# Kernel optimization log

Hardware: AMD Instinct MI355X
Metric: run time of the kernel (lower is better)

Reference implementation:

```python
import jax, jax.numpy as jnp
import numpy as np

B, N, DIM = 4, 8192, 1024
H, DH, W = 16, 64, 128
INNER = H * DH


def setup_inputs() -> dict:
    key = jax.random.key(0)
    k0, k1, k2, k3 = jax.random.split(key, 4)
    s = 0.02
    return {
        "x": jax.random.normal(k0, (B, N, DIM), jnp.float32),
        "wq": jax.random.normal(k1, (DIM, INNER), jnp.float32) * s,
        "wkv": jax.random.normal(k2, (DIM, 2 * INNER), jnp.float32) * s,
        "wo": jax.random.normal(k3, (INNER, DIM), jnp.float32) * s,
        "bo": jnp.zeros((DIM,), jnp.float32),
    }


def reference(x, wq, wkv, wo, bo):
    b, n, _ = x.shape
    h, dh, w = H, DH, W
    scale = dh ** -0.5
    # projections (n is a multiple of w, so no padding path)
    q = x @ wq
    k, v = jnp.split(x @ wkv, 2, axis=-1)

    def to_windows(t):
        # b n (h d) -> (b h) n d -> (b h) n/w w d
        t = t.reshape(b, n, h, dh).transpose(0, 2, 1, 3)
        return t.reshape(b * h, n // w, w, dh)

    qw, kw, vw = map(to_windows, (q, k, v))

    def add_prev_window(t):
        # prepend a zero window, then each window sees [prev, current] -> j = 2w
        tp = jnp.pad(t, ((0, 0), (1, 0), (0, 0), (0, 0)))
        return jnp.concatenate([tp[:, :-1], tp[:, 1:]], axis=2)

    kw, vw = add_prev_window(kw), add_prev_window(vw)

    sim = jnp.einsum('bwid,bwjd->bwij', qw, kw) * scale  # (bh, n/w, w, 2w)
    i, j = w, 2 * w
    causal = jnp.triu(jnp.ones((i, j), bool), j - i + 1)  # masks j > i + w
    neg = -jnp.finfo(sim.dtype).max
    sim = jnp.where(causal, neg, sim)
    attn = jax.nn.softmax(sim, axis=-1)
    out = jnp.einsum('bwij,bwjd->bwid', attn, vw)  # (bh, n/w, w, dh)
    out = out.reshape(b, h, n, dh).transpose(0, 2, 1, 3).reshape(b, n, h * dh)
    return out @ wo + bo
```

## Files before the change

### kernel.cpp

```cpp
#include <hip/hip_runtime.h>
#include <stdint.h>

typedef unsigned short u16;
typedef __bf16 bf16x8 __attribute__((ext_vector_type(8)));
typedef float f32x4 __attribute__((ext_vector_type(4)));
typedef unsigned short u16x8 __attribute__((ext_vector_type(8)));

#define MFMA16(a, b, c) __builtin_amdgcn_mfma_f32_16x16x32_bf16((a), (b), (c), 0, 0, 0)

#define SEQ_N 8192
#define NWIN 64

#define BAR() __builtin_amdgcn_s_barrier()
#define PRIO1() __builtin_amdgcn_s_setprio(1)
#define PRIO0() __builtin_amdgcn_s_setprio(0)
#define SB0() __builtin_amdgcn_sched_barrier(0)
#define VM8() asm volatile("s_waitcnt vmcnt(8)" ::: "memory")
#define VM0() asm volatile("s_waitcnt vmcnt(0)" ::: "memory")
#define LGKM0() asm volatile("s_waitcnt lgkmcnt(0)" ::: "memory")

__device__ __forceinline__ u16 f2bf(float f) {
  union { float f; uint32_t u; } v; v.f = f;
  return (u16)((v.u + 0x7fffu + ((v.u >> 16) & 1u)) >> 16);
}

__device__ __forceinline__ void load_lds16(const void* g, void* l) {
  __builtin_amdgcn_global_load_lds((const __attribute__((address_space(1))) void*)g,
                                   (__attribute__((address_space(3))) void*)l, 16, 0, 0);
}

__global__ __launch_bounds__(256) void cast_bf16_kernel(const float* __restrict__ src,
                                                        u16* __restrict__ dst, int n8) {
  int i = blockIdx.x * 256 + threadIdx.x;
  if (i >= n8) return;
  const float4* s = (const float4*)src + (size_t)i * 2;
  float4 a = s[0], b = s[1];
  u16x8 o;
  o[0] = f2bf(a.x); o[1] = f2bf(a.y); o[2] = f2bf(a.z); o[3] = f2bf(a.w);
  o[4] = f2bf(b.x); o[5] = f2bf(b.y); o[6] = f2bf(b.z); o[7] = f2bf(b.w);
  *((u16x8*)dst + i) = o;
}

__global__ __launch_bounds__(256) void transpose_cast_kernel(u16* __restrict__ dst,
                                                             const float* __restrict__ srcA,
                                                             const float* __restrict__ srcB,
                                                             int bcols) {
  __shared__ float tile[32][33];
  const int tx = threadIdx.x & 31, ty = threadIdx.x >> 5;
  const int n0 = blockIdx.x * 32, k0 = blockIdx.y * 32;
#pragma unroll
  for (int i = 0; i < 4; ++i) {
    int k = k0 + ty + i * 8;
    int n = n0 + tx;
    float v = (n < 1024) ? srcA[(size_t)k * 1024 + n]
                         : srcB[(size_t)k * bcols + (n - 1024)];
    tile[ty + i * 8][tx] = v;
  }
  __syncthreads();
#pragma unroll
  for (int i = 0; i < 4; ++i) {
    int n = n0 + ty + i * 8;
    int k = k0 + tx;
    dst[(size_t)n * 1024 + k] = f2bf(tile[tx][ty + i * 8]);
  }
}

#define READ_A_TO(dst, MH)                                                         \
  _Pragma("unroll") for (int kk = 0; kk < 2; ++kk)                                 \
  _Pragma("unroll") for (int m = 0; m < 4; ++m)                                    \
    dst[m][kk] = *(const bf16x8*)(Ard + bo + (((MH) * 64 + m * 16) << 7) + ax[kk]);

#define READ_B_TO(dst, NH)                                                         \
  _Pragma("unroll") for (int kk = 0; kk < 2; ++kk)                                 \
  _Pragma("unroll") for (int n = 0; n < 2; ++n)                                    \
    dst[n][kk] = *(const bf16x8*)(Brd + bo + (((NH) * 32 + n * 16) << 7) + ax[kk]);

#define MFMAQ(fa, fb, MH, NH)                                                      \
  _Pragma("unroll") for (int kk = 0; kk < 2; ++kk)                                 \
  _Pragma("unroll") for (int m = 0; m < 4; ++m)                                    \
  _Pragma("unroll") for (int n = 0; n < 2; ++n)                                    \
    acc[(MH) * 4 + m][(NH) * 2 + n] =                                              \
        MFMA16(fa[m][kk], fb[n][kk], acc[(MH) * 4 + m][(NH) * 2 + n]);

template <int NBN, int MODE>
__global__ __launch_bounds__(512, 2) void gemm8_kernel(
    const u16* __restrict__ A, const u16* __restrict__ Bt,
    u16* __restrict__ qo, u16* __restrict__ ko, u16* __restrict__ vo,
    float* __restrict__ out, const float* __restrict__ bias) {
  extern __shared__ char smem[];
  constexpr int K = 1024;
  constexpr int NT = K / 64;
  const int tid = threadIdx.x;
  const int wave = tid >> 6, lane = tid & 63;
  const int quad = lane >> 4, l15 = lane & 15;
  const int wm = wave >> 2, wn = wave & 3;

  const int idx0 = blockIdx.x;
  const int local = idx0 >> 3;
  const int bn = local >> 4;
  const int bm = ((idx0 & 7) << 4) + (local & 15);

  char* const Ab = smem;
  char* const Bb = smem + 65536;

  const int sr = lane >> 3;
  const int sg = ((lane & 7) ^ sr) * 8;
  const u16* const gA = A + (size_t)(bm * 256 + wave * 32 + sr) * K + sg;
  const u16* const gB = Bt + (size_t)(bn * 256 + wave * 32 + sr) * K + sg;
  const size_t aN = (size_t)((bm & 31) * 256 + wave * 32 + sr);
  const int ab16 = (bm >> 5) * 16;
  char* const lA = Ab + wave * 32 * 128;
  char* const lB = Bb + wave * 32 * 128;

  auto stage = [&](int buf, int kt) {
    if constexpr (MODE == 0) {
#pragma unroll
      for (int i = 0; i < 4; ++i)
        load_lds16(gA + (size_t)kt * 64 + i * 8 * K, lA + buf * 32768 + i * 1024);
    } else {
      const u16* g = A + (((size_t)(ab16 + kt)) << 19) + (aN << 6) + sg;
#pragma unroll
      for (int i = 0; i < 4; ++i)
        load_lds16(g + i * 512, lA + buf * 32768 + i * 1024);
    }
#pragma unroll
    for (int i = 0; i < 4; ++i)
      load_lds16(gB + (size_t)kt * 64 + i * 8 * K, lB + buf * 32768 + i * 1024);
  };

  const int ax[2] = { (quad ^ (l15 & 7)) << 4, ((quad ^ (l15 & 7)) << 4) ^ 64 };
  const char* const Ard = Ab + ((wm * 128 + l15) << 7);
  const char* const Brd = Bb + ((wn * 64 + l15) << 7);

  f32x4 acc[8][4] = {};
  bf16x8 afA[4][2], afB[4][2], bf0[2][2], bf1[2][2];

  stage(0, 0);
  stage(1, 1);
  VM8();
  BAR();

  for (int kt = 0; kt < NT; ++kt) {
    const int bo = (kt & 1) * 32768;
    READ_A_TO(afA, 0)
    READ_B_TO(bf0, 0)
    READ_B_TO(bf1, 1)
    SB0();
    PRIO1(); MFMAQ(afA, bf0, 0, 0) PRIO0();
    BAR();
    READ_A_TO(afB, 1)
    SB0();
    PRIO1(); MFMAQ(afA, bf1, 0, 1) PRIO0();
    BAR();
    PRIO1(); MFMAQ(afB, bf1, 1, 1) PRIO0();
    LGKM0();
    BAR();
    if (kt + 2 < NT) stage(kt & 1, kt + 2);
    PRIO1(); MFMAQ(afB, bf0, 1, 0) PRIO0();
    if (kt < NT - 1) {
      if (kt + 2 < NT) { VM8(); } else { VM0(); }
      BAR();
    }
  }

  const int row0 = bm * 256 + wm * 128;
#pragma unroll
  for (int mt = 0; mt < 8; ++mt) {
#pragma unroll
    for (int nt = 0; nt < 4; ++nt) {
      if (MODE == 0) {
        const int col = bn * 256 + wn * 64 + nt * 16 + l15;
        u16* dst = (col < 1024) ? qo : ((col < 2048) ? ko : vo);
        const int cc = col & 1023;
        const size_t hb = (((size_t)(ab16 + (cc >> 6))) << 19) + (size_t)(cc & 63);
        const int nb = (bm & 31) * 256 + wm * 128 + mt * 16 + quad * 4;
#pragma unroll
        for (int r = 0; r < 4; ++r)
          dst[hb + ((size_t)(nb + r) << 6)] = f2bf(acc[mt][nt][r]);
      } else {
        const int col = bn * 256 + wn * 64 + nt * 16 + l15;
        const float bv = bias[col];
#pragma unroll
        for (int r = 0; r < 4; ++r) {
          const int row = row0 + mt * 16 + quad * 4 + r;
          out[(size_t)row * 1024 + col] = acc[mt][nt][r] + bv;
        }
      }
    }
  }
}

__global__ __launch_bounds__(256, 2) void attn_kernel(const u16* __restrict__ qb,
                                                      const u16* __restrict__ kb,
                                                      const u16* __restrict__ vb,
                                                      u16* __restrict__ ob) {
  __shared__ u16 Vt[64][264];
  __shared__ u16 Ps[4 * 2048];
  const int tid = threadIdx.x;
  const int wave = tid >> 6, lane = tid & 63;
  const int quad = lane >> 4, l15 = lane & 15;
  const int raw = blockIdx.x;
  const int blk = ((raw & 7) << 9) | (raw >> 3);
  const int wi = blk & (NWIN - 1);
  const int bh = blk >> 6;
  const long qbase = ((long)bh * SEQ_N + (long)wi * 128) * 64;
  const long kbase = ((long)bh * SEQ_N + (long)wi * 128 - 128) * 64;

  {
    const int t = tid;
    const bool pad = (wi == 0) && (t < 128);
#pragma unroll
    for (int d0 = 0; d0 < 64; d0 += 8) {
      u16x8 v8;
      if (pad) {
        v8 = (u16x8)0;
      } else {
        v8 = *(const u16x8*)(vb + (kbase + (long)t * 64 + d0));
      }
#pragma unroll
      for (int j = 0; j < 8; ++j) Vt[d0 + j][t] = v8[j];
    }
  }

  bf16x8 qf[2][2];
#pragma unroll
  for (int mt = 0; mt < 2; ++mt)
#pragma unroll
    for (int kk = 0; kk < 2; ++kk)
      qf[mt][kk] = *(const bf16x8*)(qb + (qbase + (long)(wave * 32 + mt * 16 + l15) * 64 +
                                          kk * 32 + quad * 8));

  f32x4 s[2][16] = {};
#pragma unroll
  for (int nt = 0; nt < 16; ++nt) {
    if (!((wi == 0) && (nt < 8))) {
      const long kt = kbase + (long)(nt * 16 + l15) * 64;
      bf16x8 kf0 = *(const bf16x8*)(kb + (kt + quad * 8));
      bf16x8 kf1 = *(const bf16x8*)(kb + (kt + 32 + quad * 8));
#pragma unroll
      for (int mt = 0; mt < 2; ++mt) {
        s[mt][nt] = MFMA16(qf[mt][0], kf0, s[mt][nt]);
        s[mt][nt] = MFMA16(qf[mt][1], kf1, s[mt][nt]);
      }
    }
  }

#pragma unroll
  for (int mt = 0; mt < 2; ++mt) {
#pragma unroll
    for (int r = 0; r < 4; ++r) {
      const int row = wave * 32 + mt * 16 + quad * 4 + r;
      float m = -3.0e38f;
#pragma unroll
      for (int nt = 0; nt < 16; ++nt) {
        const int col = nt * 16 + l15;
        float x = s[mt][nt][r] * 0.125f;
        if (col > row + 128) x = -3.0e38f;
        s[mt][nt][r] = x;
        m = fmaxf(m, x);
      }
      m = fmaxf(m, __shfl_xor(m, 1));
      m = fmaxf(m, __shfl_xor(m, 2));
      m = fmaxf(m, __shfl_xor(m, 4));
      m = fmaxf(m, __shfl_xor(m, 8));
      float sum = 0.f;
#pragma unroll
      for (int nt = 0; nt < 16; ++nt) {
        float e = __expf(s[mt][nt][r] - m);
        s[mt][nt][r] = e;
        sum += e;
      }
      sum += __shfl_xor(sum, 1);
      sum += __shfl_xor(sum, 2);
      sum += __shfl_xor(sum, 4);
      sum += __shfl_xor(sum, 8);
      const float inv = 1.0f / sum;
#pragma unroll
      for (int nt = 0; nt < 16; ++nt) s[mt][nt][r] *= inv;
    }
  }

  __syncthreads();

  f32x4 o[2][4] = {};
#pragma unroll
  for (int ks = 0; ks < 8; ++ks) {
    u16* myP = &Ps[wave * 2048 + (ks & 1) * 1024];
#pragma unroll
    for (int mt = 0; mt < 2; ++mt)
#pragma unroll
      for (int half = 0; half < 2; ++half) {
        const int nt = ks * 2 + half;
#pragma unroll
        for (int r = 0; r < 4; ++r)
          myP[(mt * 16 + quad * 4 + r) * 32 + half * 16 + l15] = f2bf(s[mt][nt][r]);
      }
    bf16x8 pf[2];
    pf[0] = *(const bf16x8*)&myP[l15 * 32 + quad * 8];
    pf[1] = *(const bf16x8*)&myP[(16 + l15) * 32 + quad * 8];
#pragma unroll
    for (int ont = 0; ont < 4; ++ont) {
      bf16x8 vf = *(const bf16x8*)&Vt[ont * 16 + l15][ks * 32 + quad * 8];
      o[0][ont] = MFMA16(pf[0], vf, o[0][ont]);
      o[1][ont] = MFMA16(pf[1], vf, o[1][ont]);
    }
  }

#pragma unroll
  for (int mt = 0; mt < 2; ++mt)
#pragma unroll
    for (int ont = 0; ont < 4; ++ont)
#pragma unroll
      for (int r = 0; r < 4; ++r) {
        const int row = wave * 32 + mt * 16 + quad * 4 + r;
        const int col = ont * 16 + l15;
        ob[qbase + (long)row * 64 + col] = f2bf(o[mt][ont][r]);
      }
}

extern "C" void kernel_launch(void* const* d_in, const int* in_sizes, int n_in,
                              void* d_out, int out_size, void* d_ws, size_t ws_size,
                              hipStream_t stream) {
  const float* x   = (const float*)d_in[0];
  const float* wq  = (const float*)d_in[1];
  const float* wkv = (const float*)d_in[2];
  const float* wo  = (const float*)d_in[3];
  const float* bo  = (const float*)d_in[4];
  float* out = (float*)d_out;

  const size_t XE = (size_t)4 * SEQ_N * 1024;
  u16* ws = (u16*)d_ws;
  u16* xb    = ws;
  u16* qbuf  = ws + XE;
  u16* kbuf  = ws + 2 * XE;
  u16* vbuf  = ws + 3 * XE;
  u16* wqkvT = ws + 4 * XE;
  u16* woT   = wqkvT + 3072 * 1024;
  u16* obuf  = xb;

  hipFuncSetAttribute(reinterpret_cast<const void*>(gemm8_kernel<12, 0>),
                      hipFuncAttributeMaxDynamicSharedMemorySize, 131072);
  hipFuncSetAttribute(reinterpret_cast<const void*>(gemm8_kernel<4, 1>),
                      hipFuncAttributeMaxDynamicSharedMemorySize, 131072);

  cast_bf16_kernel<<<16384, 256, 0, stream>>>(x, xb, (int)(XE / 8));
  transpose_cast_kernel<<<dim3(96, 32), 256, 0, stream>>>(wqkvT, wq, wkv, 2048);
  transpose_cast_kernel<<<dim3(32, 32), 256, 0, stream>>>(woT, wo, wo, 1024);
  gemm8_kernel<12, 0><<<1536, 512, 131072, stream>>>(xb, wqkvT, qbuf, kbuf, vbuf,
                                                     nullptr, nullptr);
  attn_kernel<<<4096, 256, 0, stream>>>(qbuf, kbuf, vbuf, obuf);
  gemm8_kernel<4, 1><<<512, 512, 131072, stream>>>(obuf, woT, nullptr, nullptr, nullptr,
                                                   out, bo);
}
```

Baseline: 652.1 us.

## Stage K tile in LDS and XOR-swizzle V and P shared buffers

The attention kernel now copies the 256x64 K window into LDS once per block with direct global-to-LDS loads, instead of having every wave read K fragments from global memory. The padded V transpose buffer and the per-wave P staging buffer switch to XOR-swizzled layouts to cut LDS bank conflicts. The block barrier moves ahead of the QK^T loop. LDS use grows to about 80KB per block, which leaves only two blocks per CU, and the K copy for the first window now reads rows before the start of the tensor that are never used.

```diff
diff --git a/kernel.cpp b/kernel.cpp
--- a/kernel.cpp
+++ b/kernel.cpp
@@ -194,7 +194,8 @@
                                                       const u16* __restrict__ kb,
                                                       const u16* __restrict__ vb,
                                                       u16* __restrict__ ob) {
-  __shared__ u16 Vt[64][264];
+  __shared__ u16 Klds[256 * 64];
+  __shared__ u16 Vt[64 * 256];
   __shared__ u16 Ps[4 * 2048];
   const int tid = threadIdx.x;
   const int wave = tid >> 6, lane = tid & 63;
@@ -207,8 +208,18 @@
   const long kbase = ((long)bh * SEQ_N + (long)wi * 128 - 128) * 64;
 
   {
+    const int sr = lane >> 3;
+    const int sg = ((lane & 7) ^ sr) * 8;
+    const u16* g = kb + kbase + (long)(wave * 64 + sr) * 64 + sg;
+#pragma unroll
+    for (int i = 0; i < 8; ++i)
+      load_lds16(g + i * 512, Klds + (wave * 64 + i * 8) * 64);
+  }
+
+  {
     const int t = tid;
     const bool pad = (wi == 0) && (t < 128);
+    const int tg = t >> 3, t7 = t & 7;
 #pragma unroll
     for (int d0 = 0; d0 < 64; d0 += 8) {
       u16x8 v8;
@@ -218,7 +229,10 @@
         v8 = *(const u16x8*)(vb + (kbase + (long)t * 64 + d0));
       }
 #pragma unroll
-      for (int j = 0; j < 8; ++j) Vt[d0 + j][t] = v8[j];
+      for (int j = 0; j < 8; ++j) {
+        const int d = d0 + j;
+        Vt[d * 256 + (((tg ^ (d & 7)) << 3) | t7)] = v8[j];
+      }
     }
   }
 
@@ -230,13 +244,16 @@
       qf[mt][kk] = *(const bf16x8*)(qb + (qbase + (long)(wave * 32 + mt * 16 + l15) * 64 +
                                           kk * 32 + quad * 8));
 
+  __syncthreads();
+
+  const int axk = (quad ^ (l15 & 7)) << 4;
   f32x4 s[2][16] = {};
 #pragma unroll
   for (int nt = 0; nt < 16; ++nt) {
     if (!((wi == 0) && (nt < 8))) {
-      const long kt = kbase + (long)(nt * 16 + l15) * 64;
-      bf16x8 kf0 = *(const bf16x8*)(kb + (kt + quad * 8));
-      bf16x8 kf1 = *(const bf16x8*)(kb + (kt + 32 + quad * 8));
+      const char* kr = (const char*)(Klds + (nt * 16 + l15) * 64);
+      bf16x8 kf0 = *(const bf16x8*)(kr + axk);
+      bf16x8 kf1 = *(const bf16x8*)(kr + (axk ^ 64));
 #pragma unroll
       for (int mt = 0; mt < 2; ++mt) {
         s[mt][nt] = MFMA16(qf[mt][0], kf0, s[mt][nt]);
@@ -280,8 +297,6 @@
     }
   }
 
-  __syncthreads();
-
   f32x4 o[2][4] = {};
 #pragma unroll
   for (int ks = 0; ks < 8; ++ks) {
@@ -291,16 +306,20 @@
 #pragma unroll
       for (int half = 0; half < 2; ++half) {
         const int nt = ks * 2 + half;
+        const int colw = (((half * 2 + (l15 >> 3)) ^ quad) << 3) | (l15 & 7);
 #pragma unroll
         for (int r = 0; r < 4; ++r)
-          myP[(mt * 16 + quad * 4 + r) * 32 + half * 16 + l15] = f2bf(s[mt][nt][r]);
+          myP[(mt * 16 + quad * 4 + r) * 32 + colw] = f2bf(s[mt][nt][r]);
       }
     bf16x8 pf[2];
-    pf[0] = *(const bf16x8*)&myP[l15 * 32 + quad * 8];
-    pf[1] = *(const bf16x8*)&myP[(16 + l15) * 32 + quad * 8];
+#pragma unroll
+    for (int h = 0; h < 2; ++h)
+      pf[h] = *(const bf16x8*)&myP[(h * 16 + l15) * 32 +
+                                   ((quad ^ ((l15 >> 2) & 3)) << 3)];
 #pragma unroll
     for (int ont = 0; ont < 4; ++ont) {
-      bf16x8 vf = *(const bf16x8*)&Vt[ont * 16 + l15][ks * 32 + quad * 8];
+      bf16x8 vf = *(const bf16x8*)&Vt[(ont * 16 + l15) * 256 +
+                                      ((((ks * 4 + quad) ^ (l15 & 7))) << 3)];
       o[0][ont] = MFMA16(pf[0], vf, o[0][ont]);
       o[1][ont] = MFMA16(pf[1], vf, o[1][ont]);
     }
```

New measurement: 612.1 us. 6.1% less time.
